# Kernel optimization log

Hardware: AMD Instinct MI355X
Metric: run time of the kernel (lower is better)

Reference implementation:

```python
import jax, jax.numpy as jnp
import numpy as np

B, S, D, H = 8, 2048, 1024, 16
A = D // H  # attn_dim = 64
SCALE = float(np.sqrt(D))  # module divides by sqrt(d_model), NOT sqrt(attn_dim)


def setup_inputs() -> dict:
    key = jax.random.key(0)
    ks = jax.random.split(key, 6)
    # xavier-uniform bound for Linear(dim -> attn_dim)
    bound = float(np.sqrt(6.0 / (D + A)))
    return {
        "query": jax.random.normal(ks[0], (B, S, D), dtype=jnp.float32),
        "key": jax.random.normal(ks[1], (B, S, D), dtype=jnp.float32),
        "value": jax.random.normal(ks[2], (B, S, D), dtype=jnp.float32),
        "Wq": jax.random.uniform(ks[3], (D, A), jnp.float32, -bound, bound),
        "bq": jnp.zeros((A,), jnp.float32),
        "Wk": jax.random.uniform(ks[4], (D, A), jnp.float32, -bound, bound),
        "bk": jnp.zeros((A,), jnp.float32),
        "Wv": jax.random.uniform(ks[5], (D, A), jnp.float32, -bound, bound),
        "bv": jnp.zeros((A,), jnp.float32),
    }


def reference(query, key, value, Wq, bq, Wk, bk, Wv, bv):
    # Linear projections dim -> attn_dim
    q = query @ Wq + bq  # [B, S, A]
    k = key @ Wk + bk    # [B, S, A]
    v = value @ Wv + bv  # [B, S, A]
    # scaled dot-product attention; score matrix [B, S, S] is materialized
    score = jnp.einsum("bqa,bka->bqk", q, k) / SCALE
    attn = jax.nn.softmax(score, axis=-1)
    # dropout is identity in eval mode
    context = jnp.einsum("bqk,bka->bqa", attn, v)  # [B, S, A]
    return (context, attn)
```

## Files before the change

### kernel.cpp

```cpp
#include <hip/hip_runtime.h>
#include <hip/hip_bf16.h>

#define NB 8
#define SEQ 2048
#define DM 1024
#define AD 64
#define NROWS (NB * SEQ)

#define SCL2 0.04508422f

typedef __attribute__((ext_vector_type(8))) short short8;
typedef __attribute__((ext_vector_type(4))) float f32x4;

static __device__ __forceinline__ unsigned short f2bf(float f) {
    unsigned int u = __float_as_uint(f);
    u += 0x7FFFu + ((u >> 16) & 1u);
    return (unsigned short)(u >> 16);
}

static __device__ __forceinline__ f32x4 mfma16(short8 a, short8 b, f32x4 c) {
    return __builtin_amdgcn_mfma_f32_16x16x32_bf16(a, b, c, 0, 0, 0);
}

static __device__ __forceinline__ short8 pack8v(f32x4 a, f32x4 b) {
    short8 r;
    r[0] = (short)f2bf(a[0]); r[1] = (short)f2bf(a[1]);
    r[2] = (short)f2bf(a[2]); r[3] = (short)f2bf(a[3]);
    r[4] = (short)f2bf(b[0]); r[5] = (short)f2bf(b[1]);
    r[6] = (short)f2bf(b[2]); r[7] = (short)f2bf(b[3]);
    return r;
}

static __device__ __forceinline__ uint2 cvt2bf4(float4 v) {
    uint2 pk;
    pk.x = (unsigned)f2bf(v.x) | ((unsigned)f2bf(v.y) << 16);
    pk.y = (unsigned)f2bf(v.z) | ((unsigned)f2bf(v.w) << 16);
    return pk;
}

__global__ __launch_bounds__(256) void wT_kernel(
    const float* __restrict__ Wq, const float* __restrict__ Wk,
    const float* __restrict__ Wv, unsigned short* __restrict__ wT) {
    int p = blockIdx.y;
    int k0 = blockIdx.x * 64;
    const float* W = (p == 0) ? Wq : (p == 1) ? Wk : Wv;
    __shared__ unsigned short tl[64][72];
    int t = threadIdx.x;
    int c = t & 63;
    int r0 = t >> 6;
    for (int i = 0; i < 16; i++) {
        int k = r0 + i * 4;
        tl[c][k] = f2bf(W[(size_t)(k0 + k) * AD + c]);
    }
    __syncthreads();
    for (int i = 0; i < 16; i++) {
        int a = r0 + i * 4;
        wT[((size_t)p * AD + a) * DM + k0 + c] = tl[a][c];
    }
}

__global__ __launch_bounds__(128, 4) void proj_kernel(
    const float* __restrict__ q_in, const float* __restrict__ k_in,
    const float* __restrict__ v_in, const float* __restrict__ bq,
    const float* __restrict__ bk, const float* __restrict__ bv,
    const unsigned short* __restrict__ wT,
    unsigned short* __restrict__ q_out, unsigned short* __restrict__ k_out,
    unsigned short* __restrict__ vT_out) {
    int p = blockIdx.y;
    int rbase = blockIdx.x * 16;
    const float* X = (p == 0) ? q_in : (p == 1) ? k_in : v_in;
    const float* bias = (p == 0) ? bq : (p == 1) ? bk : bv;
    const unsigned short* wTp = wT + (size_t)p * AD * DM;

    __shared__ unsigned short xsb[2][16][68];
    __shared__ unsigned short wsm[2][64][68];

    int t = threadIdx.x;
    int lane = t & 63;
    int w = t >> 6;
    int arow = lane & 15;
    int agrp = lane >> 4;

    int sxrow = t >> 3;
    int sxcol = (t & 7) * 8;
    int swrow = t >> 1;
    int swcol = (t & 1) * 32;

    const float* Xb = X + (size_t)rbase * DM;

    f32x4 acc[2];
    acc[0] = (f32x4){0.f, 0.f, 0.f, 0.f};
    acc[1] = (f32x4){0.f, 0.f, 0.f, 0.f};

    float4 px0, px1;
    float4 pw0, pw1, pw2, pw3;

#define LOADSET(kb)                                                              \
    {                                                                            \
        px0 = *reinterpret_cast<const float4*>(&Xb[(size_t)sxrow * DM + (kb) + sxcol]);     \
        px1 = *reinterpret_cast<const float4*>(&Xb[(size_t)sxrow * DM + (kb) + sxcol + 4]); \
        const char* wp_ = reinterpret_cast<const char*>(&wTp[(size_t)swrow * DM + (kb) + swcol]); \
        pw0 = *reinterpret_cast<const float4*>(wp_);                             \
        pw1 = *reinterpret_cast<const float4*>(wp_ + 16);                        \
        pw2 = *reinterpret_cast<const float4*>(wp_ + 32);                        \
        pw3 = *reinterpret_cast<const float4*>(wp_ + 48);                        \
    }

#define WRITESET(bo)                                                             \
    {                                                                            \
        *reinterpret_cast<uint2*>(&xsb[bo][sxrow][sxcol]) = cvt2bf4(px0);        \
        *reinterpret_cast<uint2*>(&xsb[bo][sxrow][sxcol + 4]) = cvt2bf4(px1);    \
        *reinterpret_cast<float4*>(&wsm[bo][swrow][swcol]) = pw0;                \
        *reinterpret_cast<float4*>(&wsm[bo][swrow][swcol + 8]) = pw1;            \
        *reinterpret_cast<float4*>(&wsm[bo][swrow][swcol + 16]) = pw2;           \
        *reinterpret_cast<float4*>(&wsm[bo][swrow][swcol + 24]) = pw3;           \
    }

    LOADSET(0);
    WRITESET(0);
    __syncthreads();

    for (int c = 0; c < 16; ++c) {
        int bu = c & 1;
        if (c < 15) LOADSET((c + 1) * 64);
        const unsigned short* xr = &xsb[bu][arow][0];
#pragma unroll
        for (int s = 0; s < 2; ++s) {
            short8 af = *reinterpret_cast<const short8*>(&xr[s * 32 + agrp * 8]);
#pragma unroll
            for (int ct = 0; ct < 2; ++ct) {
                short8 bf = *reinterpret_cast<const short8*>(
                    &wsm[bu][w * 32 + ct * 16 + arow][s * 32 + agrp * 8]);
                acc[ct] = mfma16(af, bf, acc[ct]);
            }
        }
        if (c < 15) WRITESET(bu ^ 1);
        __syncthreads();
    }
#undef LOADSET
#undef WRITESET

    if (p < 2) {
        unsigned short* outp = (p == 0) ? q_out : k_out;
#pragma unroll
        for (int ct = 0; ct < 2; ct++) {
            int a = w * 32 + ct * 16 + arow;
            float bv_ = bias[a];
#pragma unroll
            for (int rr = 0; rr < 4; rr++) {
                int row = rbase + agrp * 4 + rr;
                outp[(size_t)row * AD + a] = f2bf(acc[ct][rr] + bv_);
            }
        }
    } else {
        unsigned short* sc = (unsigned short*)&xsb[0][0][0];
#pragma unroll
        for (int ct = 0; ct < 2; ct++) {
            int a = w * 32 + ct * 16 + arow;
            float bv_ = bias[a];
#pragma unroll
            for (int rr = 0; rr < 4; rr++) {
                int row = agrp * 4 + rr;
                sc[a * 20 + row] = f2bf(acc[ct][rr] + bv_);
            }
        }
        __syncthreads();
        int bidx = rbase >> 11;
        int sbase = rbase & 2047;
        int a = t >> 1;
        int sg = (t & 1) * 8;
        uint2 v0 = *reinterpret_cast<const uint2*>(&sc[a * 20 + sg]);
        uint2 v1 = *reinterpret_cast<const uint2*>(&sc[a * 20 + sg + 4]);
        unsigned short* vrow = vT_out + ((size_t)bidx * AD + a) * SEQ + sbase + sg;
        *reinterpret_cast<uint2*>(vrow) = v0;
        *reinterpret_cast<uint2*>(vrow + 4) = v1;
    }
}

__global__ __launch_bounds__(512, 2) void attn2_kernel(
    const unsigned short* __restrict__ qb, const unsigned short* __restrict__ kb,
    const unsigned short* __restrict__ vT, float* __restrict__ attn_out,
    float* __restrict__ ctx_out) {
    int blk = blockIdx.x;
    int b = blk & 7;
    int qbase = (blk >> 3) * 32;

    __shared__ float sf[8][32][68];
    __shared__ float wsum[8][32];
    __shared__ float lr_lds[32];

    int t = threadIdx.x;
    int lane = t & 63;
    int w = t >> 6;
    int arow = lane & 15;
    int agrp = lane >> 4;

    const unsigned short* qrow = qb + ((size_t)b * SEQ + qbase) * AD;
    short8 qf0a = *reinterpret_cast<const short8*>(qrow + (size_t)arow * AD + agrp * 8);
    short8 qf1a = *reinterpret_cast<const short8*>(qrow + (size_t)arow * AD + 32 + agrp * 8);
    short8 qf0b = *reinterpret_cast<const short8*>(qrow + (size_t)(16 + arow) * AD + agrp * 8);
    short8 qf1b = *reinterpret_cast<const short8*>(qrow + (size_t)(16 + arow) * AD + 32 + agrp * 8);
    const unsigned short* kbp = kb + (size_t)b * SEQ * AD;
    const unsigned short* vTb = vT + (size_t)b * AD * SEQ;
    float* attn_b = attn_out + ((size_t)b * SEQ + qbase) * SEQ;

    int keybase = w * 256;

    float sA[4] = {0.f, 0.f, 0.f, 0.f};
    float sB[4] = {0.f, 0.f, 0.f, 0.f};
    for (int kt = 0; kt < 16; ++kt) {
        int key0 = keybase + kt * 16;
        const unsigned short* krow = kbp + (size_t)(key0 + arow) * AD;
        short8 kf0 = *reinterpret_cast<const short8*>(krow + agrp * 8);
        short8 kf1 = *reinterpret_cast<const short8*>(krow + 32 + agrp * 8);
        f32x4 aA = (f32x4){0.f, 0.f, 0.f, 0.f};
        aA = mfma16(qf0a, kf0, aA);
        aA = mfma16(qf1a, kf1, aA);
        f32x4 aB = (f32x4){0.f, 0.f, 0.f, 0.f};
        aB = mfma16(qf0b, kf0, aB);
        aB = mfma16(qf1b, kf1, aB);
#pragma unroll
        for (int r = 0; r < 4; r++) {
            sA[r] += __builtin_amdgcn_exp2f(aA[r] * SCL2);
            sB[r] += __builtin_amdgcn_exp2f(aB[r] * SCL2);
        }
    }
#pragma unroll
    for (int r = 0; r < 4; r++) {
#pragma unroll
        for (int off = 1; off < 16; off <<= 1) {
            sA[r] += __shfl_xor(sA[r], off);
            sB[r] += __shfl_xor(sB[r], off);
        }
    }
    if (arow == 0) {
#pragma unroll
        for (int r = 0; r < 4; r++) {
            wsum[w][agrp * 4 + r] = sA[r];
            wsum[w][16 + agrp * 4 + r] = sB[r];
        }
    }
    __syncthreads();
    if (t < 32) {
        float S = ((wsum[0][t] + wsum[1][t]) + (wsum[2][t] + wsum[3][t])) +
                  ((wsum[4][t] + wsum[5][t]) + (wsum[6][t] + wsum[7][t]));
        lr_lds[t] = -__builtin_amdgcn_logf(S);
    }
    __syncthreads();

    float lrA[4], lrB[4];
#pragma unroll
    for (int r = 0; r < 4; r++) {
        lrA[r] = lr_lds[agrp * 4 + r];
        lrB[r] = lr_lds[16 + agrp * 4 + r];
    }

    f32x4 caccA[4], caccB[4];
#pragma unroll
    for (int ct = 0; ct < 4; ct++) {
        caccA[ct] = (f32x4){0.f, 0.f, 0.f, 0.f};
        caccB[ct] = (f32x4){0.f, 0.f, 0.f, 0.f};
    }

    for (int g = 0; g < 4; ++g) {
        int key0b = keybase + g * 64;
#pragma unroll
        for (int kb4 = 0; kb4 < 4; ++kb4) {
            int k0 = key0b + kb4 * 16;
            const unsigned short* krow = kbp + (size_t)(k0 + arow) * AD;
            short8 kf0 = *reinterpret_cast<const short8*>(krow + agrp * 8);
            short8 kf1 = *reinterpret_cast<const short8*>(krow + 32 + agrp * 8);
            f32x4 aA = (f32x4){0.f, 0.f, 0.f, 0.f};
            aA = mfma16(qf0a, kf0, aA);
            aA = mfma16(qf1a, kf1, aA);
            f32x4 aB = (f32x4){0.f, 0.f, 0.f, 0.f};
            aB = mfma16(qf0b, kf0, aB);
            aB = mfma16(qf1b, kf1, aB);
#pragma unroll
            for (int r = 0; r < 4; r++) {
                sf[w][agrp * 4 + r][kb4 * 16 + arow] =
                    __builtin_amdgcn_exp2f(aA[r] * SCL2 + lrA[r]);
                sf[w][16 + agrp * 4 + r][kb4 * 16 + arow] =
                    __builtin_amdgcn_exp2f(aB[r] * SCL2 + lrB[r]);
            }
        }
#pragma unroll
        for (int j = 0; j < 8; ++j) {
            int row = j * 4 + agrp;
            int c4 = arow * 4;
            f32x4 vv = *reinterpret_cast<const f32x4*>(&sf[w][row][c4]);
            __builtin_nontemporal_store(
                vv, reinterpret_cast<f32x4*>(&attn_b[(size_t)row * SEQ + key0b + c4]));
        }
#pragma unroll
        for (int ks = 0; ks < 2; ++ks) {
            f32x4 pa0 = *reinterpret_cast<const f32x4*>(&sf[w][arow][ks * 32 + agrp * 8]);
            f32x4 pa1 = *reinterpret_cast<const f32x4*>(&sf[w][arow][ks * 32 + agrp * 8 + 4]);
            short8 pfA = pack8v(pa0, pa1);
            f32x4 pb0 = *reinterpret_cast<const f32x4*>(&sf[w][16 + arow][ks * 32 + agrp * 8]);
            f32x4 pb1 = *reinterpret_cast<const f32x4*>(&sf[w][16 + arow][ks * 32 + agrp * 8 + 4]);
            short8 pfB = pack8v(pb0, pb1);
#pragma unroll
            for (int ct = 0; ct < 4; ct++) {
                const unsigned short* vr =
                    vTb + (size_t)(ct * 16 + arow) * SEQ + key0b + ks * 32 + agrp * 8;
                short8 vv = *reinterpret_cast<const short8*>(vr);
                caccA[ct] = mfma16(pfA, vv, caccA[ct]);
                caccB[ct] = mfma16(pfB, vv, caccB[ct]);
            }
        }
    }

    __syncthreads();
#pragma unroll
    for (int ct = 0; ct < 4; ct++)
#pragma unroll
        for (int r = 0; r < 4; r++) {
            sf[w][agrp * 4 + r][ct * 16 + arow] = caccA[ct][r];
            sf[w][16 + agrp * 4 + r][ct * 16 + arow] = caccB[ct][r];
        }
    __syncthreads();

    float* ctx_b = ctx_out + ((size_t)b * SEQ + qbase) * AD;
    for (int i = t; i < 32 * 64; i += 512) {
        int r = i >> 6, a = i & 63;
        float v = ((sf[0][r][a] + sf[1][r][a]) + (sf[2][r][a] + sf[3][r][a])) +
                  ((sf[4][r][a] + sf[5][r][a]) + (sf[6][r][a] + sf[7][r][a]));
        __builtin_nontemporal_store(v, &ctx_b[(size_t)r * AD + a]);
    }
}

extern "C" void kernel_launch(void* const* d_in, const int* in_sizes, int n_in,
                              void* d_out, int out_size, void* d_ws, size_t ws_size,
                              hipStream_t stream) {
    const float* q_in = (const float*)d_in[0];
    const float* k_in = (const float*)d_in[1];
    const float* v_in = (const float*)d_in[2];
    const float* Wq = (const float*)d_in[3];
    const float* bq = (const float*)d_in[4];
    const float* Wk = (const float*)d_in[5];
    const float* bk = (const float*)d_in[6];
    const float* Wv = (const float*)d_in[7];
    const float* bv = (const float*)d_in[8];

    char* ws = (char*)d_ws;
    unsigned short* q_bf = (unsigned short*)(ws);
    unsigned short* k_bf = (unsigned short*)(ws + (2u << 20));
    unsigned short* vT   = (unsigned short*)(ws + (4u << 20));
    unsigned short* wT   = (unsigned short*)(ws + (6u << 20));

    float* ctx_out = (float*)d_out;
    float* attn_out = ctx_out + (size_t)NB * SEQ * AD;

    hipLaunchKernelGGL(wT_kernel, dim3(16, 3), dim3(256), 0, stream, Wq, Wk, Wv, wT);
    hipLaunchKernelGGL(proj_kernel, dim3(1024, 3), dim3(128), 0, stream,
                       q_in, k_in, v_in, bq, bk, bv, wT, q_bf, k_bf, vT);
    hipLaunchKernelGGL(attn2_kernel, dim3(512), dim3(512), 0, stream,
                       q_bf, k_bf, vT, attn_out, ctx_out);
}
```

Baseline: 115.1 us.

## Pipeline projection with direct global-to-LDS loads, triple buffering, 32-row tiles

The projection kernel now issues global_load_lds (direct global-to-LDS DMA) for the fp32 X tiles and bf16 weight tiles into a three-stage ring buffer, waiting on vmcnt counters instead of staging through registers. Each block covers 32 rows instead of 16, so every weight tile read is reused across two row groups, and the grid is halved. X stays fp32 in LDS and is converted to bf16 when the MFMA operands are read. This is meant to hide memory latency and cut register-staged copies, at the cost of more LDS per block and twice the LDS read traffic for X.

After: 113.3 us. About the same (-1.5%).

```diff
diff --git a/kernel.cpp b/kernel.cpp
--- a/kernel.cpp
+++ b/kernel.cpp
@@ -11,6 +11,9 @@
 
 typedef __attribute__((ext_vector_type(8))) short short8;
 typedef __attribute__((ext_vector_type(4))) float f32x4;
+
+#define GAS __attribute__((address_space(1)))
+#define LAS __attribute__((address_space(3)))
 
 static __device__ __forceinline__ unsigned short f2bf(float f) {
     unsigned int u = __float_as_uint(f);
@@ -31,11 +34,9 @@
     return r;
 }
 
-static __device__ __forceinline__ uint2 cvt2bf4(float4 v) {
-    uint2 pk;
-    pk.x = (unsigned)f2bf(v.x) | ((unsigned)f2bf(v.y) << 16);
-    pk.y = (unsigned)f2bf(v.z) | ((unsigned)f2bf(v.w) << 16);
-    return pk;
+static __device__ __forceinline__ void gload16(const void* g, void* l) {
+    __builtin_amdgcn_global_load_lds((const GAS unsigned int*)g,
+                                     (LAS unsigned int*)l, 16, 0, 0);
 }
 
 __global__ __launch_bounds__(256) void wT_kernel(
@@ -59,7 +60,7 @@
     }
 }
 
-__global__ __launch_bounds__(128, 4) void proj_kernel(
+__global__ __launch_bounds__(128) void proj_kernel(
     const float* __restrict__ q_in, const float* __restrict__ k_in,
     const float* __restrict__ v_in, const float* __restrict__ bq,
     const float* __restrict__ bk, const float* __restrict__ bv,
@@ -67,13 +68,13 @@
     unsigned short* __restrict__ q_out, unsigned short* __restrict__ k_out,
     unsigned short* __restrict__ vT_out) {
     int p = blockIdx.y;
-    int rbase = blockIdx.x * 16;
+    int rbase = blockIdx.x * 32;
     const float* X = (p == 0) ? q_in : (p == 1) ? k_in : v_in;
     const float* bias = (p == 0) ? bq : (p == 1) ? bk : bv;
     const unsigned short* wTp = wT + (size_t)p * AD * DM;
 
-    __shared__ unsigned short xsb[2][16][68];
-    __shared__ unsigned short wsm[2][64][68];
+    __shared__ float xs[3][2048];
+    __shared__ unsigned short wsm[3][4096];
 
     int t = threadIdx.x;
     int lane = t & 63;
@@ -81,64 +82,66 @@
     int arow = lane & 15;
     int agrp = lane >> 4;
 
-    int sxrow = t >> 3;
-    int sxcol = (t & 7) * 8;
-    int swrow = t >> 1;
-    int swcol = (t & 1) * 32;
-
     const float* Xb = X + (size_t)rbase * DM;
 
-    f32x4 acc[2];
-    acc[0] = (f32x4){0.f, 0.f, 0.f, 0.f};
-    acc[1] = (f32x4){0.f, 0.f, 0.f, 0.f};
-
-    float4 px0, px1;
-    float4 pw0, pw1, pw2, pw3;
-
-#define LOADSET(kb)                                                              \
-    {                                                                            \
-        px0 = *reinterpret_cast<const float4*>(&Xb[(size_t)sxrow * DM + (kb) + sxcol]);     \
-        px1 = *reinterpret_cast<const float4*>(&Xb[(size_t)sxrow * DM + (kb) + sxcol + 4]); \
-        const char* wp_ = reinterpret_cast<const char*>(&wTp[(size_t)swrow * DM + (kb) + swcol]); \
-        pw0 = *reinterpret_cast<const float4*>(wp_);                             \
-        pw1 = *reinterpret_cast<const float4*>(wp_ + 16);                        \
-        pw2 = *reinterpret_cast<const float4*>(wp_ + 32);                        \
-        pw3 = *reinterpret_cast<const float4*>(wp_ + 48);                        \
-    }
-
-#define WRITESET(bo)                                                             \
-    {                                                                            \
-        *reinterpret_cast<uint2*>(&xsb[bo][sxrow][sxcol]) = cvt2bf4(px0);        \
-        *reinterpret_cast<uint2*>(&xsb[bo][sxrow][sxcol + 4]) = cvt2bf4(px1);    \
-        *reinterpret_cast<float4*>(&wsm[bo][swrow][swcol]) = pw0;                \
-        *reinterpret_cast<float4*>(&wsm[bo][swrow][swcol + 8]) = pw1;            \
-        *reinterpret_cast<float4*>(&wsm[bo][swrow][swcol + 16]) = pw2;           \
-        *reinterpret_cast<float4*>(&wsm[bo][swrow][swcol + 24]) = pw3;           \
-    }
-
-    LOADSET(0);
-    WRITESET(0);
-    __syncthreads();
-
+#define STAGE(c, bu)                                                         \
+    {                                                                        \
+        _Pragma("unroll") for (int i = 0; i < 4; ++i) {                      \
+            int rg_ = i * 2 + w;                                             \
+            int row_ = rg_ * 4 + (lane >> 4);                                \
+            gload16(Xb + (size_t)row_ * DM + (c) * 64 + (lane & 15) * 4,     \
+                    &xs[bu][rg_ * 256 + lane * 4]);                          \
+            int wr_ = rg_ * 8 + (lane >> 3);                                 \
+            gload16(wTp + (size_t)wr_ * DM + (c) * 64 + (lane & 7) * 8,      \
+                    &wsm[bu][rg_ * 512 + lane * 8]);                         \
+        }                                                                    \
+    }
+
+    f32x4 acc00 = (f32x4){0.f, 0.f, 0.f, 0.f};
+    f32x4 acc01 = (f32x4){0.f, 0.f, 0.f, 0.f};
+    f32x4 acc10 = (f32x4){0.f, 0.f, 0.f, 0.f};
+    f32x4 acc11 = (f32x4){0.f, 0.f, 0.f, 0.f};
+
+#define COMPUTE(bu)                                                          \
+    {                                                                        \
+        const float* xr0 = &xs[bu][(size_t)(0 + arow) * 64];                 \
+        const float* xr1 = &xs[bu][(size_t)(16 + arow) * 64];                \
+        _Pragma("unroll") for (int s = 0; s < 2; ++s) {                      \
+            f32x4 a00 = *reinterpret_cast<const f32x4*>(&xr0[s * 32 + agrp * 8]);     \
+            f32x4 a01 = *reinterpret_cast<const f32x4*>(&xr0[s * 32 + agrp * 8 + 4]); \
+            short8 af0 = pack8v(a00, a01);                                   \
+            f32x4 a10 = *reinterpret_cast<const f32x4*>(&xr1[s * 32 + agrp * 8]);     \
+            f32x4 a11 = *reinterpret_cast<const f32x4*>(&xr1[s * 32 + agrp * 8 + 4]); \
+            short8 af1 = pack8v(a10, a11);                                   \
+            short8 bf0 = *reinterpret_cast<const short8*>(                   \
+                &wsm[bu][(size_t)(w * 32 + arow) * 64 + s * 32 + agrp * 8]); \
+            short8 bf1 = *reinterpret_cast<const short8*>(                   \
+                &wsm[bu][(size_t)(w * 32 + 16 + arow) * 64 + s * 32 + agrp * 8]); \
+            acc00 = mfma16(af0, bf0, acc00);                                 \
+            acc01 = mfma16(af0, bf1, acc01);                                 \
+            acc10 = mfma16(af1, bf0, acc10);                                 \
+            acc11 = mfma16(af1, bf1, acc11);                                 \
+        }                                                                    \
+    }
+
+    STAGE(0, 0);
+    STAGE(1, 1);
+    int bu = 0, bs = 2;
     for (int c = 0; c < 16; ++c) {
-        int bu = c & 1;
-        if (c < 15) LOADSET((c + 1) * 64);
-        const unsigned short* xr = &xsb[bu][arow][0];
-#pragma unroll
-        for (int s = 0; s < 2; ++s) {
-            short8 af = *reinterpret_cast<const short8*>(&xr[s * 32 + agrp * 8]);
-#pragma unroll
-            for (int ct = 0; ct < 2; ++ct) {
-                short8 bf = *reinterpret_cast<const short8*>(
-                    &wsm[bu][w * 32 + ct * 16 + arow][s * 32 + agrp * 8]);
-                acc[ct] = mfma16(af, bf, acc[ct]);
-            }
-        }
-        if (c < 15) WRITESET(bu ^ 1);
-        __syncthreads();
-    }
-#undef LOADSET
-#undef WRITESET
+        if (c + 2 < 16) STAGE(c + 2, bs);
+        if (c < 14)
+            asm volatile("s_waitcnt vmcnt(16)\n\ts_barrier" ::: "memory");
+        else if (c == 14)
+            asm volatile("s_waitcnt vmcnt(8)\n\ts_barrier" ::: "memory");
+        else
+            asm volatile("s_waitcnt vmcnt(0)\n\ts_barrier" ::: "memory");
+        COMPUTE(bu);
+        asm volatile("s_barrier" ::: "memory");
+        bu = (bu == 2) ? 0 : bu + 1;
+        bs = (bs == 2) ? 0 : bs + 1;
+    }
+#undef STAGE
+#undef COMPUTE
 
     if (p < 2) {
         unsigned short* outp = (p == 0) ? q_out : k_out;
@@ -148,32 +151,41 @@
             float bv_ = bias[a];
 #pragma unroll
             for (int rr = 0; rr < 4; rr++) {
-                int row = rbase + agrp * 4 + rr;
-                outp[(size_t)row * AD + a] = f2bf(acc[ct][rr] + bv_);
+                int r0 = rbase + agrp * 4 + rr;
+                int r1 = rbase + 16 + agrp * 4 + rr;
+                float v0 = (ct == 0) ? acc00[rr] : acc01[rr];
+                float v1 = (ct == 0) ? acc10[rr] : acc11[rr];
+                outp[(size_t)r0 * AD + a] = f2bf(v0 + bv_);
+                outp[(size_t)r1 * AD + a] = f2bf(v1 + bv_);
             }
         }
     } else {
-        unsigned short* sc = (unsigned short*)&xsb[0][0][0];
+        unsigned short* sc = (unsigned short*)&xs[0][0];
 #pragma unroll
         for (int ct = 0; ct < 2; ct++) {
             int a = w * 32 + ct * 16 + arow;
             float bv_ = bias[a];
 #pragma unroll
             for (int rr = 0; rr < 4; rr++) {
-                int row = agrp * 4 + rr;
-                sc[a * 20 + row] = f2bf(acc[ct][rr] + bv_);
+                int r0 = agrp * 4 + rr;
+                int r1 = 16 + agrp * 4 + rr;
+                float v0 = (ct == 0) ? acc00[rr] : acc01[rr];
+                float v1 = (ct == 0) ? acc10[rr] : acc11[rr];
+                sc[a * 40 + r0] = f2bf(v0 + bv_);
+                sc[a * 40 + r1] = f2bf(v1 + bv_);
             }
         }
         __syncthreads();
         int bidx = rbase >> 11;
         int sbase = rbase & 2047;
         int a = t >> 1;
-        int sg = (t & 1) * 8;
-        uint2 v0 = *reinterpret_cast<const uint2*>(&sc[a * 20 + sg]);
-        uint2 v1 = *reinterpret_cast<const uint2*>(&sc[a * 20 + sg + 4]);
+        int sg = (t & 1) * 16;
         unsigned short* vrow = vT_out + ((size_t)bidx * AD + a) * SEQ + sbase + sg;
-        *reinterpret_cast<uint2*>(vrow) = v0;
-        *reinterpret_cast<uint2*>(vrow + 4) = v1;
+#pragma unroll
+        for (int i = 0; i < 4; i++) {
+            uint2 v = *reinterpret_cast<const uint2*>(&sc[a * 40 + sg + i * 4]);
+            *reinterpret_cast<uint2*>(vrow + i * 4) = v;
+        }
     }
 }
 
@@ -353,7 +365,7 @@
     float* attn_out = ctx_out + (size_t)NB * SEQ * AD;
 
     hipLaunchKernelGGL(wT_kernel, dim3(16, 3), dim3(256), 0, stream, Wq, Wk, Wv, wT);
-    hipLaunchKernelGGL(proj_kernel, dim3(1024, 3), dim3(128), 0, stream,
+    hipLaunchKernelGGL(proj_kernel, dim3(512, 3), dim3(128), 0, stream,
                        q_in, k_in, v_in, bq, bk, bv, wT, q_bf, k_bf, vT);
     hipLaunchKernelGGL(attn2_kernel, dim3(512), dim3(512), 0, stream,
                        q_bf, k_bf, vT, attn_out, ctx_out);
```
